# Kernel optimization log

Measured on AMD Instinct MI355X. Metric: run time of the kernel, lower is better.

The kernel has to match this reference:

```python
import jax, jax.numpy as jnp
import numpy as np

TOP_K = 2
NORM_TOPK_PROB = True


def setup_inputs() -> dict:
    key = jax.random.key(0)
    k1, k2 = jax.random.split(key)
    hidden_states = jax.random.normal(k1, (4, 4096, 2048), dtype=jnp.float32)
    # gate weight [n_routed_experts, hidden_size], kaiming-uniform-like scale
    weight = jax.random.normal(k2, (64, 2048), dtype=jnp.float32) * 0.02
    return {"hidden_states": hidden_states, "weight": weight}


def reference(hidden_states, weight):
    bsz, seq_len, h = hidden_states.shape
    x = hidden_states.reshape(-1, h)                      # [T, H]
    logits = jnp.einsum("th,eh->te", x, weight)           # [T, E]
    scores = jax.nn.softmax(logits, axis=-1)              # [T, E]
    topk_weight, topk_idx = jax.lax.top_k(scores, TOP_K)  # [T, K] each
    if TOP_K > 1 and NORM_TOPK_PROB:
        topk_weight = topk_weight / (topk_weight.sum(axis=-1, keepdims=True) + 1e-20)
    return (topk_idx.reshape(bsz, seq_len, -1), topk_weight.reshape(bsz, seq_len, -1))
```

## Files before the change

kernel.cpp:

```cpp
#include <hip/hip_runtime.h>
#include <math.h>

#define H    2048
#define NE   64
#define TOKB 64
#define KC   32
#define NCH  (H / KC)
#define NBUF 3
#define TAU  4.0e-3f
#define NEGF (-3.0e38f)

typedef __bf16 bf16x8 __attribute__((ext_vector_type(8)));
typedef float  f32x16 __attribute__((ext_vector_type(16)));

#define MFMA(a, b, c) __builtin_amdgcn_mfma_f32_32x32x16_bf16((a), (b), (c), 0, 0, 0)
#define LD4(p) (*reinterpret_cast<const float4*>(p))

__device__ __forceinline__ void cvt8(const float4 a, const float4 b,
                                     bf16x8& hi, bf16x8& lo) {
    const float v0 = a.x, v1 = a.y, v2 = a.z, v3 = a.w;
    const float v4 = b.x, v5 = b.y, v6 = b.z, v7 = b.w;
    hi[0] = (__bf16)v0; lo[0] = (__bf16)(v0 - (float)hi[0]);
    hi[1] = (__bf16)v1; lo[1] = (__bf16)(v1 - (float)hi[1]);
    hi[2] = (__bf16)v2; lo[2] = (__bf16)(v2 - (float)hi[2]);
    hi[3] = (__bf16)v3; lo[3] = (__bf16)(v3 - (float)hi[3]);
    hi[4] = (__bf16)v4; lo[4] = (__bf16)(v4 - (float)hi[4]);
    hi[5] = (__bf16)v5; lo[5] = (__bf16)(v5 - (float)hi[5]);
    hi[6] = (__bf16)v6; lo[6] = (__bf16)(v6 - (float)hi[6]);
    hi[7] = (__bf16)v7; lo[7] = (__bf16)(v7 - (float)hi[7]);
}

__device__ __forceinline__ void gll16(const float* g, float* l) {
    __builtin_amdgcn_global_load_lds(
        (const __attribute__((address_space(1))) void*)g,
        (__attribute__((address_space(3))) void*)l, 16, 0, 0);
}

__global__ void zero_wl(int* __restrict__ wl) {
    if (threadIdx.x == 0) wl[0] = 0;
}

__global__ __launch_bounds__(256) void moe_gate_mfma(
    const float* __restrict__ x,
    const float* __restrict__ w,
    float* __restrict__ out,
    int woff,
    int* __restrict__ wl, int wlcap)
{
    __shared__ float lds[NBUF][4096];

    const int tid  = threadIdx.x;
    const int lane = tid & 63;
    const int wv   = tid >> 6;
    const int mt   = wv >> 1;
    const int kh   = wv & 1;
    const int lo5  = lane & 31;
    const int hi5  = lane >> 5;
    const int t0   = blockIdx.x * TOKB;

    const float* sbase[4];
    #pragma unroll
    for (int s = 0; s < 4; ++s) {
        const int idx = (wv * 4 + s) * 256 + lane * 4;
        const int tr  = (idx & 2047) >> 5;
        const int sl  = ((idx >> 2) & 7) ^ (tr & 7);
        sbase[s] = (idx < 2048)
            ? (w + (size_t)tr * H + sl * 4)
            : (x + (size_t)(t0 + tr) * H + sl * 4);
    }

    f32x16 acc0, acc1;
    #pragma unroll
    for (int i = 0; i < 16; ++i) { acc0[i] = 0.f; acc1[i] = 0.f; }

    #pragma unroll
    for (int s = 0; s < 4; ++s) gll16(sbase[s],      &lds[0][(wv * 4 + s) * 256]);
    #pragma unroll
    for (int s = 0; s < 4; ++s) gll16(sbase[s] + KC, &lds[1][(wv * 4 + s) * 256]);

    const int s0  = kh * 4 + hi5 * 2;
    const int xk  = lo5 & 7;
    const int rb  = mt * 32 + lo5;
    const int ra0 = lo5, ra1 = 32 + lo5;
    const int obB  = 2048 + rb * 32;
    const int obA0 = ra0 * 32, obA1 = ra1 * 32;
    const int c0 = ((s0)     ^ xk) << 2;
    const int c1 = ((s0 + 1) ^ xk) << 2;

    int ib = 0, iw = 2;
    for (int c = 0; c < NCH; ++c) {
        if (c < NCH - 1) {
            asm volatile("s_waitcnt vmcnt(4)" ::: "memory");
        } else {
            asm volatile("s_waitcnt vmcnt(0)" ::: "memory");
        }
        __builtin_amdgcn_s_barrier();

        const float* buf = lds[ib];
        const float4 b1  = LD4(&buf[obB  + c0]);
        const float4 b2  = LD4(&buf[obB  + c1]);
        const float4 a01 = LD4(&buf[obA0 + c0]);
        const float4 a02 = LD4(&buf[obA0 + c1]);
        const float4 a11 = LD4(&buf[obA1 + c0]);
        const float4 a12 = LD4(&buf[obA1 + c1]);

        bf16x8 bh, bl, ah0, al0, ah1, al1;
        cvt8(b1, b2, bh, bl);
        cvt8(a01, a02, ah0, al0);
        cvt8(a11, a12, ah1, al1);

        acc0 = MFMA(ah0, bh, acc0);
        acc1 = MFMA(ah1, bh, acc1);
        acc0 = MFMA(ah0, bl, acc0);
        acc1 = MFMA(ah1, bl, acc1);
        acc0 = MFMA(al0, bh, acc0);
        acc1 = MFMA(al1, bh, acc1);

        if (c + 2 < NCH) {
            const int kc = (c + 2) * KC;
            #pragma unroll
            for (int s = 0; s < 4; ++s)
                gll16(sbase[s] + kc, &lds[iw][(wv * 4 + s) * 256]);
        }
        ib = (ib == NBUF - 1) ? 0 : ib + 1;
        iw = (iw == NBUF - 1) ? 0 : iw + 1;
    }

    __syncthreads();
    float* S = &lds[0][0];
    if (kh == 1) {
        const int base = (mt * 32 + lo5) * 65;
        #pragma unroll
        for (int r = 0; r < 16; ++r) {
            const int e0 = (r & 3) + 8 * (r >> 2) + 4 * hi5;
            S[base + e0]      = acc0[r];
            S[base + 32 + e0] = acc1[r];
        }
    }
    __syncthreads();
    if (kh == 1) return;
    {
        const int base = (mt * 32 + lo5) * 65;
        #pragma unroll
        for (int r = 0; r < 16; ++r) {
            const int e0 = (r & 3) + 8 * (r >> 2) + 4 * hi5;
            acc0[r] += S[base + e0];
            acc1[r] += S[base + 32 + e0];
        }
    }

    float m1 = NEGF, m2 = NEGF, m3 = NEGF;
    int   i1 = 0, i2 = 0;
    #pragma unroll
    for (int r = 0; r < 16; ++r) {
        const float v = acc0[r];
        const int   e = (r & 3) + 8 * (r >> 2) + 4 * hi5;
        if (v > m1)      { m3 = m2; m2 = m1; i2 = i1; m1 = v; i1 = e; }
        else if (v > m2) { m3 = m2; m2 = v; i2 = e; }
        else if (v > m3) { m3 = v; }
    }
    #pragma unroll
    for (int r = 0; r < 16; ++r) {
        const float v = acc1[r];
        const int   e = 32 + (r & 3) + 8 * (r >> 2) + 4 * hi5;
        if (v > m1)      { m3 = m2; m2 = m1; i2 = i1; m1 = v; i1 = e; }
        else if (v > m2) { m3 = m2; m2 = v; i2 = e; }
        else if (v > m3) { m3 = v; }
    }

    const float n1 = __shfl_xor(m1, 32), n2 = __shfl_xor(m2, 32), n3 = __shfl_xor(m3, 32);
    const int   j1 = __shfl_xor(i1, 32), j2 = __shfl_xor(i2, 32);

    float a1, a2, a3, b1, b2, b3; int ia1, ia2, ib1, ib2;
    const bool aF = (m1 > n1) || (m1 == n1 && i1 < j1);
    if (aF) { a1=m1; a2=m2; a3=m3; ia1=i1; ia2=i2; b1=n1; b2=n2; b3=n3; ib1=j1; ib2=j2; }
    else    { a1=n1; a2=n2; a3=n3; ia1=j1; ia2=j2; b1=m1; b2=m2; b3=m3; ib1=i1; ib2=i2; }

    const float o1 = a1; const int oi1 = ia1;
    float o2, o3; int oi2;
    const bool a2F = (a2 > b1) || (a2 == b1 && ia2 < ib1);
    if (a2F) { o2 = a2; oi2 = ia2; o3 = (a3 > b1) ? a3 : b1; }
    else     { o2 = b1; oi2 = ib1; o3 = (a2 > b2) ? a2 : b2; }

    if (hi5 == 0) {
        const int t = t0 + mt * 32 + lo5;
        const float r = expf(o2 - o1);
        const float s = 1.0f + r;
        out[2 * t + 0]        = (float)oi1;
        out[2 * t + 1]        = (float)oi2;
        out[woff + 2 * t + 0] = 1.0f / s;
        out[woff + 2 * t + 1] = r / s;
        if ((o1 - o2 < TAU) || (o2 - o3 < TAU)) {
            const int pos = atomicAdd(wl, 1);
            if (pos < wlcap) wl[1 + pos] = t;
        }
    }
}

__global__ __launch_bounds__(256) void moe_refine_fp64(
    const float* __restrict__ x, const float* __restrict__ w,
    float* __restrict__ out, int woff,
    const int* __restrict__ wl, int wlcap)
{
    __shared__ double Sd[3][NE];
    const int lane = threadIdx.x & 63;
    const int wv   = threadIdx.x >> 6;
    const int ks   = wv * 512;
    int cnt = wl[0];
    if (cnt > wlcap) cnt = wlcap;

    for (int i = blockIdx.x; i < cnt; i += gridDim.x) {
        const int t = wl[1 + i];

        const float4 xa = LD4(&x[(size_t)t * H + ks + lane * 4]);
        const float4 xb = LD4(&x[(size_t)t * H + ks + 256 + lane * 4]);
        const double x0 = xa.x, x1 = xa.y, x2 = xa.z, x3 = xa.w;
        const double x4 = xb.x, x5 = xb.y, x6 = xb.z, x7 = xb.w;

        double myacc = 0.0;
        #pragma unroll 4
        for (int e = 0; e < NE; ++e) {
            const float4 wa = LD4(&w[(size_t)e * H + ks + lane * 4]);
            const float4 wb = LD4(&w[(size_t)e * H + ks + 256 + lane * 4]);
            double sA = 0.0, sB = 0.0;
            sA = fma((double)wa.x, x0, sA); sA = fma((double)wa.y, x1, sA);
            sA = fma((double)wa.z, x2, sA); sA = fma((double)wa.w, x3, sA);
            sB = fma((double)wb.x, x4, sB); sB = fma((double)wb.y, x5, sB);
            sB = fma((double)wb.z, x6, sB); sB = fma((double)wb.w, x7, sB);
            double s = sA + sB;
            #pragma unroll
            for (int off = 1; off < 64; off <<= 1)
                s += __shfl_xor(s, off);
            if (lane == e) myacc = s;
        }

        if (wv > 0) Sd[wv - 1][lane] = myacc;
        __syncthreads();
        if (wv == 0) {
            const double acc = ((myacc + Sd[0][lane]) + Sd[1][lane]) + Sd[2][lane];

            double v = acc; int bi = lane;
            #pragma unroll
            for (int off = 32; off > 0; off >>= 1) {
                double ov = __shfl_xor(v, off);
                int    oi = __shfl_xor(bi, off);
                if (ov > v || (ov == v && oi < bi)) { v = ov; bi = oi; }
            }
            const double m1 = v; const int i1 = bi;

            double v2 = (lane == i1) ? -1.0e300 : acc; int b2 = lane;
            #pragma unroll
            for (int off = 32; off > 0; off >>= 1) {
                double ov = __shfl_xor(v2, off);
                int    oi = __shfl_xor(b2, off);
                if (ov > v2 || (ov == v2 && oi < b2)) { v2 = ov; b2 = oi; }
            }
            const double m2 = v2; const int i2 = b2;

            if (lane == 0) {
                const double r = exp(m2 - m1);
                const double s = 1.0 + r;
                out[2 * t + 0]        = (float)i1;
                out[2 * t + 1]        = (float)i2;
                out[woff + 2 * t + 0] = (float)(1.0 / s);
                out[woff + 2 * t + 1] = (float)(r / s);
            }
        }
        __syncthreads();
    }
}

extern "C" void kernel_launch(void* const* d_in, const int* in_sizes, int n_in,
                              void* d_out, int out_size, void* d_ws, size_t ws_size,
                              hipStream_t stream) {
    const float* x   = (const float*)d_in[0];
    const float* wgt = (const float*)d_in[1];
    float* out = (float*)d_out;

    const int T    = in_sizes[0] / H;
    const int woff = out_size / 2;

    int* wl = (int*)d_ws;
    int wlcap = (int)(ws_size / sizeof(int)) - 1;
    if (wlcap > T) wlcap = T;

    zero_wl<<<dim3(1), dim3(64), 0, stream>>>(wl);

    moe_gate_mfma<<<dim3(T / TOKB), dim3(256), 0, stream>>>(
        x, wgt, out, woff, wl, wlcap);

    moe_refine_fp64<<<dim3(512), dim3(256), 0, stream>>>(
        x, wgt, out, woff, wl, wlcap);
}
```

Before: 64.66 us.

## Pre-split gate weights into bf16 hi/lo and halve token tile per block

A new prep kernel converts the gate weights once per call into interleaved bf16 hi/lo pairs in workspace, so the main kernel loads ready-made A fragments instead of converting fp32 weights in every block. The token tile drops from 64 to 32, which doubles the grid, and the waves are remapped to split experts by K-half with a single accumulator each. Top-k selection now runs from a shared-memory row per token. The cost is an extra kernel launch and more blocks re-reading the weights. The workspace sizing assumes at least 128KB plus the packed weights, and wlcap is no longer bounded by the available workspace.

```diff
diff --git a/kernel.cpp b/kernel.cpp
--- a/kernel.cpp
+++ b/kernel.cpp
@@ -3,9 +3,9 @@
 
 #define H    2048
 #define NE   64
-#define TOKB 64
+#define TOKB 32
 #define KC   32
-#define NCH  (H / KC)
+#define NCH  64
 #define NBUF 3
 #define TAU  4.0e-3f
 #define NEGF (-3.0e38f)
@@ -30,167 +30,149 @@
     hi[7] = (__bf16)v7; lo[7] = (__bf16)(v7 - (float)hi[7]);
 }
 
-__device__ __forceinline__ void gll16(const float* g, float* l) {
+__device__ __forceinline__ void gll16(const void* g, void* l) {
     __builtin_amdgcn_global_load_lds(
         (const __attribute__((address_space(1))) void*)g,
         (__attribute__((address_space(3))) void*)l, 16, 0, 0);
 }
 
-__global__ void zero_wl(int* __restrict__ wl) {
-    if (threadIdx.x == 0) wl[0] = 0;
+__global__ __launch_bounds__(256) void prep_w(
+    const float* __restrict__ w, __bf16* __restrict__ wp, int* __restrict__ wl)
+{
+    const int e   = blockIdx.x;
+    const int tid = threadIdx.x;
+    if (e == 0 && tid == 0) wl[0] = 0;
+    const float4 a = LD4(&w[e * H + tid * 8]);
+    const float4 b = LD4(&w[e * H + tid * 8 + 4]);
+    bf16x8 hi, lo;
+    cvt8(a, b, hi, lo);
+    const int c  = tid >> 2;
+    const int kk = (tid & 3) * 8;
+    *reinterpret_cast<bf16x8*>(wp + e * 4096 + c * 64 + kk)      = hi;
+    *reinterpret_cast<bf16x8*>(wp + e * 4096 + c * 64 + 32 + kk) = lo;
 }
 
 __global__ __launch_bounds__(256) void moe_gate_mfma(
     const float* __restrict__ x,
-    const float* __restrict__ w,
-    float* __restrict__ out,
-    int woff,
+    const __bf16* __restrict__ wp,
+    float* __restrict__ out, int woff,
     int* __restrict__ wl, int wlcap)
 {
-    __shared__ float lds[NBUF][4096];
+    __shared__ float4 lds4[NBUF][768];
 
     const int tid  = threadIdx.x;
     const int lane = tid & 63;
     const int wv   = tid >> 6;
-    const int mt   = wv >> 1;
-    const int kh   = wv & 1;
+    const int et   = wv >> 1;
+    const int kq   = wv & 1;
     const int lo5  = lane & 31;
     const int hi5  = lane >> 5;
     const int t0   = blockIdx.x * TOKB;
 
-    const float* sbase[4];
-    #pragma unroll
-    for (int s = 0; s < 4; ++s) {
-        const int idx = (wv * 4 + s) * 256 + lane * 4;
-        const int tr  = (idx & 2047) >> 5;
-        const int sl  = ((idx >> 2) & 7) ^ (tr & 7);
-        sbase[s] = (idx < 2048)
-            ? (w + (size_t)tr * H + sl * 4)
-            : (x + (size_t)(t0 + tr) * H + sl * 4);
-    }
-
-    f32x16 acc0, acc1;
-    #pragma unroll
-    for (int i = 0; i < 16; ++i) { acc0[i] = 0.f; acc1[i] = 0.f; }
-
-    #pragma unroll
-    for (int s = 0; s < 4; ++s) gll16(sbase[s],      &lds[0][(wv * 4 + s) * 256]);
-    #pragma unroll
-    for (int s = 0; s < 4; ++s) gll16(sbase[s] + KC, &lds[1][(wv * 4 + s) * 256]);
-
-    const int s0  = kh * 4 + hi5 * 2;
-    const int xk  = lo5 & 7;
-    const int rb  = mt * 32 + lo5;
-    const int ra0 = lo5, ra1 = 32 + lo5;
-    const int obB  = 2048 + rb * 32;
-    const int obA0 = ra0 * 32, obA1 = ra1 * 32;
-    const int c0 = ((s0)     ^ xk) << 2;
-    const int c1 = ((s0 + 1) ^ xk) << 2;
+    const char* sbase[3];
+    #pragma unroll
+    for (int s = 0; s < 3; ++s) {
+        const int byte = (s * 256 + tid) * 16;
+        if (byte < 8192) {
+            const int row = byte >> 7;
+            const int sl  = ((byte >> 4) & 7) ^ (row & 7);
+            sbase[s] = (const char*)wp + (size_t)row * 8192 + sl * 16;
+        } else {
+            const int b   = byte - 8192;
+            const int row = b >> 7;
+            const int sl  = ((b >> 4) & 7) ^ (row & 7);
+            sbase[s] = (const char*)x + (size_t)(t0 + row) * 8192 + sl * 16;
+        }
+    }
+
+    f32x16 acc;
+    #pragma unroll
+    for (int i = 0; i < 16; ++i) acc[i] = 0.f;
+
+    #pragma unroll
+    for (int s = 0; s < 3; ++s) gll16(sbase[s],       &lds4[0][s * 256 + wv * 64]);
+    #pragma unroll
+    for (int s = 0; s < 3; ++s) gll16(sbase[s] + 128, &lds4[1][s * 256 + wv * 64]);
+
+    const int ra     = et * 32 + lo5;
+    const int sA     = kq * 2 + hi5;
+    const int offAhi = ra * 128 + (((sA)     ^ (ra & 7)) << 4);
+    const int offAlo = ra * 128 + (((4 + sA) ^ (ra & 7)) << 4);
+    const int rb     = lo5;
+    const int sB     = kq * 4 + hi5 * 2;
+    const int offB0  = 8192 + rb * 128 + (((sB)     ^ (rb & 7)) << 4);
+    const int offB1  = 8192 + rb * 128 + (((sB + 1) ^ (rb & 7)) << 4);
 
     int ib = 0, iw = 2;
     for (int c = 0; c < NCH; ++c) {
         if (c < NCH - 1) {
-            asm volatile("s_waitcnt vmcnt(4)" ::: "memory");
+            asm volatile("s_waitcnt vmcnt(3)" ::: "memory");
         } else {
             asm volatile("s_waitcnt vmcnt(0)" ::: "memory");
         }
         __builtin_amdgcn_s_barrier();
 
-        const float* buf = lds[ib];
-        const float4 b1  = LD4(&buf[obB  + c0]);
-        const float4 b2  = LD4(&buf[obB  + c1]);
-        const float4 a01 = LD4(&buf[obA0 + c0]);
-        const float4 a02 = LD4(&buf[obA0 + c1]);
-        const float4 a11 = LD4(&buf[obA1 + c0]);
-        const float4 a12 = LD4(&buf[obA1 + c1]);
-
-        bf16x8 bh, bl, ah0, al0, ah1, al1;
+        const char* bufb = (const char*)&lds4[ib][0];
+        const bf16x8 ahi = *reinterpret_cast<const bf16x8*>(bufb + offAhi);
+        const bf16x8 alo = *reinterpret_cast<const bf16x8*>(bufb + offAlo);
+        const float4 b1  = *reinterpret_cast<const float4*>(bufb + offB0);
+        const float4 b2  = *reinterpret_cast<const float4*>(bufb + offB1);
+
+        bf16x8 bh, bl;
         cvt8(b1, b2, bh, bl);
-        cvt8(a01, a02, ah0, al0);
-        cvt8(a11, a12, ah1, al1);
-
-        acc0 = MFMA(ah0, bh, acc0);
-        acc1 = MFMA(ah1, bh, acc1);
-        acc0 = MFMA(ah0, bl, acc0);
-        acc1 = MFMA(ah1, bl, acc1);
-        acc0 = MFMA(al0, bh, acc0);
-        acc1 = MFMA(al1, bh, acc1);
 
         if (c + 2 < NCH) {
-            const int kc = (c + 2) * KC;
-            #pragma unroll
-            for (int s = 0; s < 4; ++s)
-                gll16(sbase[s] + kc, &lds[iw][(wv * 4 + s) * 256]);
-        }
+            #pragma unroll
+            for (int s = 0; s < 3; ++s)
+                gll16(sbase[s] + (c + 2) * 128, &lds4[iw][s * 256 + wv * 64]);
+        }
+
+        acc = MFMA(ahi, bh, acc);
+        acc = MFMA(ahi, bl, acc);
+        acc = MFMA(alo, bh, acc);
+
         ib = (ib == NBUF - 1) ? 0 : ib + 1;
         iw = (iw == NBUF - 1) ? 0 : iw + 1;
     }
 
     __syncthreads();
-    float* S = &lds[0][0];
-    if (kh == 1) {
-        const int base = (mt * 32 + lo5) * 65;
+    float* S = reinterpret_cast<float*>(&lds4[0][0]);
+    if (kq == 0) {
         #pragma unroll
         for (int r = 0; r < 16; ++r) {
-            const int e0 = (r & 3) + 8 * (r >> 2) + 4 * hi5;
-            S[base + e0]      = acc0[r];
-            S[base + 32 + e0] = acc1[r];
+            const int e = et * 32 + (r & 3) + 8 * (r >> 2) + 4 * hi5;
+            S[lo5 * 65 + e] = acc[r];
         }
     }
     __syncthreads();
-    if (kh == 1) return;
-    {
-        const int base = (mt * 32 + lo5) * 65;
+    if (kq == 1) {
         #pragma unroll
         for (int r = 0; r < 16; ++r) {
-            const int e0 = (r & 3) + 8 * (r >> 2) + 4 * hi5;
-            acc0[r] += S[base + e0];
-            acc1[r] += S[base + 32 + e0];
-        }
-    }
-
-    float m1 = NEGF, m2 = NEGF, m3 = NEGF;
-    int   i1 = 0, i2 = 0;
-    #pragma unroll
-    for (int r = 0; r < 16; ++r) {
-        const float v = acc0[r];
-        const int   e = (r & 3) + 8 * (r >> 2) + 4 * hi5;
-        if (v > m1)      { m3 = m2; m2 = m1; i2 = i1; m1 = v; i1 = e; }
-        else if (v > m2) { m3 = m2; m2 = v; i2 = e; }
-        else if (v > m3) { m3 = v; }
-    }
-    #pragma unroll
-    for (int r = 0; r < 16; ++r) {
-        const float v = acc1[r];
-        const int   e = 32 + (r & 3) + 8 * (r >> 2) + 4 * hi5;
-        if (v > m1)      { m3 = m2; m2 = m1; i2 = i1; m1 = v; i1 = e; }
-        else if (v > m2) { m3 = m2; m2 = v; i2 = e; }
-        else if (v > m3) { m3 = v; }
-    }
-
-    const float n1 = __shfl_xor(m1, 32), n2 = __shfl_xor(m2, 32), n3 = __shfl_xor(m3, 32);
-    const int   j1 = __shfl_xor(i1, 32), j2 = __shfl_xor(i2, 32);
-
-    float a1, a2, a3, b1, b2, b3; int ia1, ia2, ib1, ib2;
-    const bool aF = (m1 > n1) || (m1 == n1 && i1 < j1);
-    if (aF) { a1=m1; a2=m2; a3=m3; ia1=i1; ia2=i2; b1=n1; b2=n2; b3=n3; ib1=j1; ib2=j2; }
-    else    { a1=n1; a2=n2; a3=n3; ia1=j1; ia2=j2; b1=m1; b2=m2; b3=m3; ib1=i1; ib2=i2; }
-
-    const float o1 = a1; const int oi1 = ia1;
-    float o2, o3; int oi2;
-    const bool a2F = (a2 > b1) || (a2 == b1 && ia2 < ib1);
-    if (a2F) { o2 = a2; oi2 = ia2; o3 = (a3 > b1) ? a3 : b1; }
-    else     { o2 = b1; oi2 = ib1; o3 = (a2 > b2) ? a2 : b2; }
-
-    if (hi5 == 0) {
-        const int t = t0 + mt * 32 + lo5;
-        const float r = expf(o2 - o1);
+            const int e = et * 32 + (r & 3) + 8 * (r >> 2) + 4 * hi5;
+            S[lo5 * 65 + e] += acc[r];
+        }
+    }
+    __syncthreads();
+
+    if (tid < TOKB) {
+        const float* row = &S[tid * 65];
+        float m1 = NEGF, m2 = NEGF, m3 = NEGF;
+        int   i1 = 0, i2 = 0;
+        #pragma unroll
+        for (int e = 0; e < NE; ++e) {
+            const float v = row[e];
+            if (v > m1)      { m3 = m2; m2 = m1; i2 = i1; m1 = v; i1 = e; }
+            else if (v > m2) { m3 = m2; m2 = v; i2 = e; }
+            else if (v > m3) { m3 = v; }
+        }
+        const float r = expf(m2 - m1);
         const float s = 1.0f + r;
-        out[2 * t + 0]        = (float)oi1;
-        out[2 * t + 1]        = (float)oi2;
+        const int   t = t0 + tid;
+        out[2 * t + 0]        = (float)i1;
+        out[2 * t + 1]        = (float)i2;
         out[woff + 2 * t + 0] = 1.0f / s;
         out[woff + 2 * t + 1] = r / s;
-        if ((o1 - o2 < TAU) || (o2 - o3 < TAU)) {
+        if ((m1 - m2 < TAU) || (m2 - m3 < TAU)) {
             const int pos = atomicAdd(wl, 1);
             if (pos < wlcap) wl[1 + pos] = t;
         }
@@ -280,14 +262,15 @@
     const int T    = in_sizes[0] / H;
     const int woff = out_size / 2;
 
-    int* wl = (int*)d_ws;
-    int wlcap = (int)(ws_size / sizeof(int)) - 1;
-    if (wlcap > T) wlcap = T;
-
-    zero_wl<<<dim3(1), dim3(64), 0, stream>>>(wl);
+    int*    wl = (int*)d_ws;
+    __bf16* wp = (__bf16*)((char*)d_ws + 131072);
+    int wlcap = T;
+    if ((size_t)(131072) > ws_size) wlcap = 0;
+
+    prep_w<<<dim3(NE), dim3(256), 0, stream>>>(wgt, wp, wl);
 
     moe_gate_mfma<<<dim3(T / TOKB), dim3(256), 0, stream>>>(
-        x, wgt, out, woff, wl, wlcap);
+        x, wp, out, woff, wl, wlcap);
 
     moe_refine_fp64<<<dim3(512), dim3(256), 0, stream>>>(
         x, wgt, out, woff, wl, wlcap);
```

Result: slower. 77.14 us (+19.3%).

## Pre-split gate weights into bf16 hi/lo and deepen LDS pipeline to four buffers

Applied to the files above, without the earlier changes.

A new prep kernel converts the fp32 gate weight into pre-split bf16 hi/lo chunks once per call, replacing the zero_wl kernel. The main kernel then streams these bf16 weights directly into LDS and only converts the activation tiles in the loop. This removes the per-block weight conversion work. The LDS ring grows to four buffers with a three-chunk prefetch depth, which uses more LDS per block. The worklist capacity is now fixed to T and the weight copy sits at a fixed 128KB offset in the workspace, which assumes the workspace is large enough.

```diff
diff --git a/kernel.cpp b/kernel.cpp
--- a/kernel.cpp
+++ b/kernel.cpp
@@ -5,8 +5,8 @@
 #define NE   64
 #define TOKB 64
 #define KC   32
-#define NCH  (H / KC)
-#define NBUF 3
+#define NCH  64
+#define NBUF 4
 #define TAU  4.0e-3f
 #define NEGF (-3.0e38f)
 
@@ -30,24 +30,35 @@
     hi[7] = (__bf16)v7; lo[7] = (__bf16)(v7 - (float)hi[7]);
 }
 
-__device__ __forceinline__ void gll16(const float* g, float* l) {
+__device__ __forceinline__ void gll16(const void* g, void* l) {
     __builtin_amdgcn_global_load_lds(
         (const __attribute__((address_space(1))) void*)g,
         (__attribute__((address_space(3))) void*)l, 16, 0, 0);
 }
 
-__global__ void zero_wl(int* __restrict__ wl) {
-    if (threadIdx.x == 0) wl[0] = 0;
+__global__ __launch_bounds__(256) void prep_w(
+    const float* __restrict__ w, __bf16* __restrict__ wp, int* __restrict__ wl)
+{
+    const int e   = blockIdx.x;
+    const int tid = threadIdx.x;
+    if (e == 0 && tid == 0) wl[0] = 0;
+    const float4 a = LD4(&w[e * H + tid * 8]);
+    const float4 b = LD4(&w[e * H + tid * 8 + 4]);
+    bf16x8 hi, lo;
+    cvt8(a, b, hi, lo);
+    const int c  = tid >> 2;
+    const int kk = (tid & 3) * 8;
+    *reinterpret_cast<bf16x8*>(wp + e * 4096 + c * 64 + kk)      = hi;
+    *reinterpret_cast<bf16x8*>(wp + e * 4096 + c * 64 + 32 + kk) = lo;
 }
 
 __global__ __launch_bounds__(256) void moe_gate_mfma(
     const float* __restrict__ x,
-    const float* __restrict__ w,
-    float* __restrict__ out,
-    int woff,
+    const __bf16* __restrict__ wp,
+    float* __restrict__ out, int woff,
     int* __restrict__ wl, int wlcap)
 {
-    __shared__ float lds[NBUF][4096];
+    __shared__ float4 lds4[NBUF][1024];
 
     const int tid  = threadIdx.x;
     const int lane = tid & 63;
@@ -58,15 +69,20 @@
     const int hi5  = lane >> 5;
     const int t0   = blockIdx.x * TOKB;
 
-    const float* sbase[4];
+    const char* sbase[4];
     #pragma unroll
     for (int s = 0; s < 4; ++s) {
-        const int idx = (wv * 4 + s) * 256 + lane * 4;
-        const int tr  = (idx & 2047) >> 5;
-        const int sl  = ((idx >> 2) & 7) ^ (tr & 7);
-        sbase[s] = (idx < 2048)
-            ? (w + (size_t)tr * H + sl * 4)
-            : (x + (size_t)(t0 + tr) * H + sl * 4);
+        const int byte = (s * 256 + tid) * 16;
+        if (byte < 8192) {
+            const int row = byte >> 7;
+            const int sl  = ((byte >> 4) & 7) ^ (row & 7);
+            sbase[s] = (const char*)wp + (size_t)row * 8192 + sl * 16;
+        } else {
+            const int b   = byte - 8192;
+            const int row = b >> 7;
+            const int sl  = ((b >> 4) & 7) ^ (row & 7);
+            sbase[s] = (const char*)x + (size_t)(t0 + row) * 8192 + sl * 16;
+        }
     }
 
     f32x16 acc0, acc1;
@@ -74,40 +90,42 @@
     for (int i = 0; i < 16; ++i) { acc0[i] = 0.f; acc1[i] = 0.f; }
 
     #pragma unroll
-    for (int s = 0; s < 4; ++s) gll16(sbase[s],      &lds[0][(wv * 4 + s) * 256]);
-    #pragma unroll
-    for (int s = 0; s < 4; ++s) gll16(sbase[s] + KC, &lds[1][(wv * 4 + s) * 256]);
-
-    const int s0  = kh * 4 + hi5 * 2;
-    const int xk  = lo5 & 7;
+    for (int p = 0; p < 3; ++p)
+        #pragma unroll
+        for (int s = 0; s < 4; ++s)
+            gll16(sbase[s] + p * 128, &lds4[p][s * 256 + wv * 64]);
+
+    const int ra0 = lo5, ra1 = 32 + lo5;
+    const int sA  = kh * 2 + hi5;
+    const int offAh0 = ra0 * 128 + (((sA)     ^ (ra0 & 7)) << 4);
+    const int offAl0 = ra0 * 128 + (((4 + sA) ^ (ra0 & 7)) << 4);
+    const int offAh1 = ra1 * 128 + (((sA)     ^ (ra1 & 7)) << 4);
+    const int offAl1 = ra1 * 128 + (((4 + sA) ^ (ra1 & 7)) << 4);
     const int rb  = mt * 32 + lo5;
-    const int ra0 = lo5, ra1 = 32 + lo5;
-    const int obB  = 2048 + rb * 32;
-    const int obA0 = ra0 * 32, obA1 = ra1 * 32;
-    const int c0 = ((s0)     ^ xk) << 2;
-    const int c1 = ((s0 + 1) ^ xk) << 2;
-
-    int ib = 0, iw = 2;
+    const int sB  = kh * 4 + hi5 * 2;
+    const int offB0 = 8192 + rb * 128 + (((sB)     ^ (rb & 7)) << 4);
+    const int offB1 = 8192 + rb * 128 + (((sB + 1) ^ (rb & 7)) << 4);
+
     for (int c = 0; c < NCH; ++c) {
-        if (c < NCH - 1) {
+        if (c < NCH - 2) {
+            asm volatile("s_waitcnt vmcnt(8)" ::: "memory");
+        } else if (c == NCH - 2) {
             asm volatile("s_waitcnt vmcnt(4)" ::: "memory");
         } else {
             asm volatile("s_waitcnt vmcnt(0)" ::: "memory");
         }
         __builtin_amdgcn_s_barrier();
 
-        const float* buf = lds[ib];
-        const float4 b1  = LD4(&buf[obB  + c0]);
-        const float4 b2  = LD4(&buf[obB  + c1]);
-        const float4 a01 = LD4(&buf[obA0 + c0]);
-        const float4 a02 = LD4(&buf[obA0 + c1]);
-        const float4 a11 = LD4(&buf[obA1 + c0]);
-        const float4 a12 = LD4(&buf[obA1 + c1]);
-
-        bf16x8 bh, bl, ah0, al0, ah1, al1;
+        const char* bufb = (const char*)&lds4[c & 3][0];
+        const bf16x8 ah0 = *reinterpret_cast<const bf16x8*>(bufb + offAh0);
+        const bf16x8 al0 = *reinterpret_cast<const bf16x8*>(bufb + offAl0);
+        const bf16x8 ah1 = *reinterpret_cast<const bf16x8*>(bufb + offAh1);
+        const bf16x8 al1 = *reinterpret_cast<const bf16x8*>(bufb + offAl1);
+        const float4 b1  = *reinterpret_cast<const float4*>(bufb + offB0);
+        const float4 b2  = *reinterpret_cast<const float4*>(bufb + offB1);
+
+        bf16x8 bh, bl;
         cvt8(b1, b2, bh, bl);
-        cvt8(a01, a02, ah0, al0);
-        cvt8(a11, a12, ah1, al1);
 
         acc0 = MFMA(ah0, bh, acc0);
         acc1 = MFMA(ah1, bh, acc1);
@@ -116,18 +134,16 @@
         acc0 = MFMA(al0, bh, acc0);
         acc1 = MFMA(al1, bh, acc1);
 
-        if (c + 2 < NCH) {
-            const int kc = (c + 2) * KC;
+        if (c + 3 < NCH) {
             #pragma unroll
             for (int s = 0; s < 4; ++s)
-                gll16(sbase[s] + kc, &lds[iw][(wv * 4 + s) * 256]);
-        }
-        ib = (ib == NBUF - 1) ? 0 : ib + 1;
-        iw = (iw == NBUF - 1) ? 0 : iw + 1;
+                gll16(sbase[s] + (c + 3) * 128,
+                      &lds4[(c + 3) & 3][s * 256 + wv * 64]);
+        }
     }
 
     __syncthreads();
-    float* S = &lds[0][0];
+    float* S = reinterpret_cast<float*>(&lds4[0][0]);
     if (kh == 1) {
         const int base = (mt * 32 + lo5) * 65;
         #pragma unroll
@@ -280,14 +296,14 @@
     const int T    = in_sizes[0] / H;
     const int woff = out_size / 2;
 
-    int* wl = (int*)d_ws;
-    int wlcap = (int)(ws_size / sizeof(int)) - 1;
-    if (wlcap > T) wlcap = T;
-
-    zero_wl<<<dim3(1), dim3(64), 0, stream>>>(wl);
+    int*    wl = (int*)d_ws;
+    __bf16* wp = (__bf16*)((char*)d_ws + 131072);
+    int wlcap = T;
+
+    prep_w<<<dim3(NE), dim3(256), 0, stream>>>(wgt, wp, wl);
 
     moe_gate_mfma<<<dim3(T / TOKB), dim3(256), 0, stream>>>(
-        x, wgt, out, woff, wl, wlcap);
+        x, wp, out, woff, wl, wlcap);
 
     moe_refine_fp64<<<dim3(512), dim3(256), 0, stream>>>(
         x, wgt, out, woff, wl, wlcap);
```

Measured after the change: 73.41 us. 13.5% more time.
